# Performance work log

Measured on AMD Instinct MI355X. Metric: run time of the kernel, lower is better.

The kernel has to match this reference:

```python
import jax, jax.numpy as jnp
import numpy as np

D_MODEL = 96
D_STATE = 16
D_CONV = 3
D_INNER = 192          # expand * d_model
DT_RANK = 6            # ceil(d_model / 16)
K = 4                  # 4 scan directions
LN_EPS = 1e-5


def setup_inputs() -> dict:
    key = jax.random.key(0)
    ks = jax.random.split(key, 8)
    rn = lambda k, shape, s: jax.random.normal(k, shape, jnp.float32) * s
    return {
        "x": rn(ks[0], (8, 64, 64, D_MODEL), 1.0),
        "in_proj_w": rn(ks[1], (2 * D_INNER, D_MODEL), 0.05),
        "conv_w": rn(ks[2], (D_INNER, 1, D_CONV, D_CONV), 0.1),
        "conv_b": rn(ks[3], (D_INNER,), 0.1),
        "x_proj_w": rn(ks[4], (K * (DT_RANK + 2 * D_STATE), D_INNER), 0.05),
        "dt_projs_w": rn(ks[5], (K * D_INNER, DT_RANK), 0.1),
        "dt_projs_b": rn(ks[6], (K * D_INNER,), 0.1),
        "A_log": jnp.log(jnp.tile(jnp.arange(1, D_STATE + 1, dtype=jnp.float32), (D_INNER, 1))),
        "Ds": jnp.ones((K * D_INNER,), jnp.float32),
        "out_norm_w": jnp.ones((D_INNER,), jnp.float32),
        "out_norm_b": jnp.zeros((D_INNER,), jnp.float32),
        "out_proj_w": rn(ks[7], (D_MODEL, D_INNER), 0.05),
    }


def _selective_scan(u, delta, A, Bs, Cs):
    # u, delta: (B,K,D,L); A: (D,N); Bs, Cs: (B,K,N,L)
    Bsz = u.shape[0]

    def step(h, t):
        u_t, d_t, B_t, C_t = t                       # (B,K,D), (B,K,D), (B,K,N), (B,K,N)
        h = jnp.exp(d_t[..., None] * A) * h + (d_t * u_t)[..., None] * B_t[:, :, None, :]
        y = jnp.einsum('bkdn,bkn->bkd', h, C_t)
        return h, y

    h0 = jnp.zeros((Bsz, K, D_INNER, D_STATE), u.dtype)
    seq = (jnp.moveaxis(u, -1, 0), jnp.moveaxis(delta, -1, 0),
           jnp.moveaxis(Bs, -1, 0), jnp.moveaxis(Cs, -1, 0))
    _, ys = jax.lax.scan(step, h0, seq)
    return jnp.moveaxis(ys, 0, -1)                   # (B,K,D,L)


def reference(x, in_proj_w, conv_w, conv_b, x_proj_w, dt_projs_w, dt_projs_b,
              A_log, Ds, out_norm_w, out_norm_b, out_proj_w):
    B, H, W, C = x.shape
    L = H * W
    # in_proj + gate split
    xz = x @ in_proj_w.T                             # (B,H,W,2*D_INNER)
    x_, z = jnp.split(xz, 2, axis=-1)
    # depthwise conv + SiLU (NCHW)
    xc = jnp.transpose(x_, (0, 3, 1, 2))
    pad = (D_CONV - 1) // 2
    xc = jax.lax.conv_general_dilated(xc, conv_w, (1, 1), [(pad, pad), (pad, pad)],
                                      feature_group_count=D_INNER)
    xc = xc + conv_b[None, :, None, None]
    xc = xc * jax.nn.sigmoid(xc)
    # CrossScan: 4 directions
    x0 = xc.reshape(B, D_INNER, L)
    x1 = jnp.transpose(xc, (0, 1, 3, 2)).reshape(B, D_INNER, L)
    xs = jnp.stack([x0, x1, x0[..., ::-1], x1[..., ::-1]], axis=1)   # (B,4,D,L)
    # per-direction projections
    x_dbl = jnp.einsum('bkdl,kcd->bkcl', xs, x_proj_w.reshape(K, -1, D_INNER))
    dts, Bs, Cs = jnp.split(x_dbl, [DT_RANK, DT_RANK + D_STATE], axis=2)
    dts = jnp.einsum('bkrl,kdr->bkdl', dts, dt_projs_w.reshape(K, D_INNER, DT_RANK))
    delta = jax.nn.softplus(dts + dt_projs_b.reshape(1, K, D_INNER, 1))
    A = -jnp.exp(A_log)                              # (D,N), shared across K
    ys = _selective_scan(xs, delta, A, Bs, Cs)
    ys = ys + Ds.reshape(1, K, D_INNER, 1) * xs      # skip term D*u
    # CrossMerge
    y02 = ys[:, 0] + ys[:, 2, :, ::-1]
    y13 = ys[:, 1] + ys[:, 3, :, ::-1]
    y = y02 + jnp.transpose(y13.reshape(B, D_INNER, W, H), (0, 1, 3, 2)).reshape(B, D_INNER, L)
    # LayerNorm over channels (out_norm, 'v0' path)
    yt = jnp.transpose(y, (0, 2, 1))                 # (B,L,D)
    mu = yt.mean(-1, keepdims=True)
    var = yt.var(-1, keepdims=True)
    yt = (yt - mu) / jnp.sqrt(var + LN_EPS) * out_norm_w + out_norm_b
    yt = yt.reshape(B, H, W, D_INNER)
    # gate and out_proj
    yg = yt * (z * jax.nn.sigmoid(z))
    return yg @ out_proj_w.T
```

## Files before the change

### kernel.cpp

```cpp
#include <hip/hip_runtime.h>
#include <hip/hip_bf16.h>

typedef __hip_bfloat16 bf16;
typedef unsigned short u16;
typedef unsigned int   u32;

constexpr int Hn=64, Wn=64, Cm=96, Ln=4096, Di=192, Kn=4, Ns=16, Rr=6;
constexpr int Gc=64, CH=64;

typedef __attribute__((ext_vector_type(8))) short bf16x8;
typedef __attribute__((ext_vector_type(4))) float f32x4;

static __device__ __forceinline__ float ldv(const float* p, long i){ return p[i]; }
static __device__ __forceinline__ float ldv(const bf16*  p, long i){ return __bfloat162float(p[i]); }
static __device__ __forceinline__ void  stv(float* p, long i, float v){ p[i] = v; }
static __device__ __forceinline__ void  stv(bf16*  p, long i, float v){ p[i] = __float2bfloat16(v); }
static __device__ __forceinline__ float bfr(u16 u){ return __uint_as_float((u32)u << 16); }
static __device__ __forceinline__ u16   fbr(float f){ bf16 h = __float2bfloat16(f); return *(u16*)&h; }
static __device__ __forceinline__ float4 ldv4(const float* p, long i){ return *(const float4*)(p + i); }
static __device__ __forceinline__ float4 ldv4(const bf16* p, long i){
  ushort4 u = *(const ushort4*)(p + i);
  return make_float4(bfr(u.x), bfr(u.y), bfr(u.z), bfr(u.w));
}
static __device__ __forceinline__ float splus(float x){ return (x > 15.f) ? x : log1pf(__expf(x)); }

static __device__ __forceinline__ bf16x8 ldb8(const float* p){
  float4 a = *(const float4*)p;
  float4 b = *(const float4*)(p + 4);
  bf16x8 r;
  r[0]=(short)fbr(a.x); r[1]=(short)fbr(a.y); r[2]=(short)fbr(a.z); r[3]=(short)fbr(a.w);
  r[4]=(short)fbr(b.x); r[5]=(short)fbr(b.y); r[6]=(short)fbr(b.z); r[7]=(short)fbr(b.w);
  return r;
}
static __device__ __forceinline__ bf16x8 ldb8(const bf16* p){
  return *(const bf16x8*)p;
}
static __device__ __forceinline__ void st8(u16* dst, const float* src){
  float4 a = *(const float4*)src;
  float4 b = *(const float4*)(src + 4);
  dst[0]=fbr(a.x); dst[1]=fbr(a.y); dst[2]=fbr(a.z); dst[3]=fbr(a.w);
  dst[4]=fbr(b.x); dst[5]=fbr(b.y); dst[6]=fbr(b.z); dst[7]=fbr(b.w);
// ... 206 lines not shown
      int b  = (int)(q >> 12);
      int ql = (int)(q & 4095);
      int l  = (k >= 2) ? (4095 - ql) : ql;
      long base = ((long)(b*4 + k))*4096 + l;
      if (t < 6){
        dtsg[base*6 + t] = fbr(acc[f][r]);
      } else {
        int n = t - 6;
        u32 v = (u32)fbr(acc[f][r]) | ((u32)fbr(acc[f+1][r]) << 16);
        BCg[base*16 + n] = v;
      }
    }
  }
}
__global__ __launch_bounds__(256) void k_proj(const u16* xcLD, const u16* xcTLD, const void* xpw,
                                              u16* dtsg, u32* BCg, const int* flag){
  __shared__ u16 sA[64*200];
  if (*flag) proj_body<float>(xcLD, xcTLD, (const float*)xpw, dtsg, BCg, sA);
  else       proj_body<bf16 >(xcLD, xcTLD, (const bf16* )xpw, dtsg, BCg, sA);
}

static __device__ __forceinline__ void sp_decay(float xv, float& dl, float& rr){
  if (xv > 15.f){ dl = xv; rr = __expf(-xv); }
  else {
    float o = 1.f + __expf(xv);
    dl = __logf(o);
    rr = __builtin_amdgcn_rcpf(o);
  }
}

__global__ __launch_bounds__(192,3) void k_scan1_fast(const u16* xcLD, const u16* xcTLD,
                                                      const u16* dtsg, const u32* BCg,
                                                      const void* dtw, const void* dtb,
                                                      float* Sb, float* Qb,
                                                      const int* flag, const int* flag2){
  if (!(*flag && *flag2)) return;
  __shared__ float sdt[384];
  __shared__ float sB[1024];
  const float* dtwf = (const float*)dtw;
  const float* dtbf = (const float*)dtb;
  int tid = threadIdx.x, blk = blockIdx.x;
  int g = blk & (Gc-1); int k = (blk >> 6) & 3; int b = blk >> 8;
  bool rev = k >= 2, odd = k & 1;
  int d = tid;
  const u16* src = (odd ? xcTLD : xcLD) + (long)b*Ln*Di;
  const u16* dlg = dtsg + (long)(b*Kn + k)*Ln*6;
  const u32* bcg = BCg + (long)(b*Kn + k)*Ln*16;
  float w[6], h[16];
  #pragma unroll
  for (int r = 0; r < 6; ++r) w[r] = dtwf[((long)k*Di + d)*6 + r];
  float bias = dtbf[k*Di + d];
  #pragma unroll
  for (int n = 0; n < 16; ++n) h[n] = 0.f;
  float S = 0.f;
  int l0 = g*CH;
  for (int i = tid; i < 48; i += 192){
    const u16* sp8 = dlg + (long)l0*6 + i*8;
    ushort4 v0 = *(const ushort4*)sp8;
    ushort4 v1 = *(const ushort4*)(sp8 + 4);
    float* dp = &sdt[i*8];
    dp[0]=bfr(v0.x); dp[1]=bfr(v0.y); dp[2]=bfr(v0.z); dp[3]=bfr(v0.w);
    dp[4]=bfr(v1.x); dp[5]=bfr(v1.y); dp[6]=bfr(v1.z); dp[7]=bfr(v1.w);
  }
  for (int i = tid; i < 256; i += 192){
    uint4 v = *(const uint4*)(bcg + (long)l0*16 + i*4);
    sB[i*4+0] = bfr((u16)(v.x & 0xffff));
    sB[i*4+1] = bfr((u16)(v.y & 0xffff));
    sB[i*4+2] = bfr((u16)(v.z & 0xffff));
    sB[i*4+3] = bfr((u16)(v.w & 0xffff));
  }
  __syncthreads();
  for (int jb = 0; jb < CH; jb += 8){
    float uv[8];
    #pragma unroll
    for (int q = 0; q < 8; ++q){
      int l = l0 + jb + q; int pos = rev ? (Ln-1-l) : l;
      uv[q] = bfr(src[(long)pos*Di + d]);
    }
    #pragma unroll
    for (int q = 0; q < 8; ++q){
      int j = jb + q;
      float xv = bias;
      #pragma unroll
      for (int r = 0; r < 6; ++r) xv += w[r]*sdt[j*6 + r];
      float dl, rr; sp_decay(xv, dl, rr);
      float du = dl * uv[q];
      float Bv[16];
      *(float4*)&Bv[0]  = *(const float4*)&sB[j*16];
      *(float4*)&Bv[4]  = *(const float4*)&sB[j*16+4];
      *(float4*)&Bv[8]  = *(const float4*)&sB[j*16+8];
      *(float4*)&Bv[12] = *(const float4*)&sB[j*16+12];
      float r2 = rr*rr, r3 = r2*rr, r4 = r2*r2, r8 = r4*r4, r12 = r8*r4;
      float S4[4] = {rr, r2, r3, r4};
      float B4[4] = {1.f, r4, r8, r12};
      #pragma unroll
      for (int n = 0; n < 16; ++n)
        h[n] = (B4[n>>2]*S4[n&3])*h[n] + du*Bv[n];
      S += dl;
    }
  }
  long ci = (long)(b*Kn + k)*Gc + g;
  Sb[ci*Di + d] = S;
  float4* qp = (float4*)(Qb + ci*3072 + (long)d*16);
  qp[0] = make_float4(h[0], h[1], h[2], h[3]);
  qp[1] = make_float4(h[4], h[5], h[6], h[7]);
  qp[2] = make_float4(h[8], h[9], h[10], h[11]);
  qp[3] = make_float4(h[12], h[13], h[14], h[15]);
}

template<typename T>
__device__ void scan1_body(const u16* xcLD, const u16* xcTLD, const u16* dtsg, const u32* BCg,
                           const T* Alog, const T* dtw, const T* dtb,
                           float* Sb, float* Qb, float* sdt, float* sB, int fastA){
  int tid = threadIdx.x, blk = blockIdx.x;
  int g = blk & (Gc-1); int k = (blk >> 6) & 3; int b = blk >> 8;
  bool rev = k >= 2, odd = k & 1;
  int d = tid;
  const u16* src = (odd ? xcTLD : xcLD) + (long)b*Ln*Di;
  const u16* dlg = dtsg + (long)(b*Kn + k)*Ln*6;
  const u32* bcg = BCg + (long)(b*Kn + k)*Ln*16;
  float w[6], h[16], a[16];
  #pragma unroll
  for (int r = 0; r < 6; ++r) w[r] = ldv(dtw, ((long)k*Di + d)*6 + r);
  float bias = ldv(dtb, k*Di + d);
  #pragma unroll
  for (int n = 0; n < 16; ++n) h[n] = 0.f;
  if (!fastA){
    #pragma unroll
    for (int n = 0; n < 16; ++n) a[n] = -__expf(ldv(Alog, (long)d*16 + n));
  }
  float S = 0.f;
  int l0 = g*CH;
  for (int i = tid; i < 48; i += 192){
    const u16* sp8 = dlg + (long)l0*6 + i*8;
    ushort4 v0 = *(const ushort4*)sp8;
    ushort4 v1 = *(const ushort4*)(sp8 + 4);
    float* dp = &sdt[i*8];
    dp[0]=bfr(v0.x); dp[1]=bfr(v0.y); dp[2]=bfr(v0.z); dp[3]=bfr(v0.w);
    dp[4]=bfr(v1.x); dp[5]=bfr(v1.y); dp[6]=bfr(v1.z); dp[7]=bfr(v1.w);
  }
  for (int i = tid; i < 256; i += 192){
    uint4 v = *(const uint4*)(bcg + (long)l0*16 + i*4);
    sB[i*4+0] = bfr((u16)(v.x & 0xffff));
    sB[i*4+1] = bfr((u16)(v.y & 0xffff));
    sB[i*4+2] = bfr((u16)(v.z & 0xffff));
    sB[i*4+3] = bfr((u16)(v.w & 0xffff));
  }
  __syncthreads();
  if (fastA){
    for (int jb = 0; jb < CH; jb += 8){
      float uv[8];
      #pragma unroll
      for (int q = 0; q < 8; ++q){
        int l = l0 + jb + q; int pos = rev ? (Ln-1-l) : l;
        uv[q] = bfr(src[(long)pos*Di + d]);
      }
      #pragma unroll
      for (int q = 0; q < 8; ++q){
        int j = jb + q;
        float xv = bias;
        #pragma unroll
        for (int r = 0; r < 6; ++r) xv += w[r]*sdt[j*6 + r];
        float dl, rr; sp_decay(xv, dl, rr);
        float du = dl * uv[q];
        float Bv[16];
        *(float4*)&Bv[0]  = *(const float4*)&sB[j*16];
        *(float4*)&Bv[4]  = *(const float4*)&sB[j*16+4];
        *(float4*)&Bv[8]  = *(const float4*)&sB[j*16+8];
        *(float4*)&Bv[12] = *(const float4*)&sB[j*16+12];
        float r2 = rr*rr, r3 = r2*rr, r4 = r2*r2, r8 = r4*r4, r12 = r8*r4;
        float S4[4] = {rr, r2, r3, r4};
        float B4[4] = {1.f, r4, r8, r12};
        #pragma unroll
        for (int n = 0; n < 16; ++n)
          h[n] = (B4[n>>2]*S4[n&3])*h[n] + du*Bv[n];
        S += dl;
      }
    }
  } else {
    for (int jb = 0; jb < CH; jb += 8){
      float uv[8];
      #pragma unroll
      for (int q = 0; q < 8; ++q){
        int l = l0 + jb + q; int pos = rev ? (Ln-1-l) : l;
        uv[q] = bfr(src[(long)pos*Di + d]);
      }
      #pragma unroll
      for (int q = 0; q < 8; ++q){
        int j = jb + q;
        float dl = bias;
        #pragma unroll
        for (int r = 0; r < 6; ++r) dl += w[r]*sdt[j*6 + r];
        dl = splus(dl);
        float du = dl * uv[q];
        float Bv[16];
        *(float4*)&Bv[0]  = *(const float4*)&sB[j*16];
        *(float4*)&Bv[4]  = *(const float4*)&sB[j*16+4];
        *(float4*)&Bv[8]  = *(const float4*)&sB[j*16+8];
        *(float4*)&Bv[12] = *(const float4*)&sB[j*16+12];
        #pragma unroll
        for (int n = 0; n < 16; ++n) h[n] = __expf(dl*a[n])*h[n] + du*Bv[n];
        S += dl;
      }
    }
  }
  long ci = (long)(b*Kn + k)*Gc + g;
  Sb[ci*Di + d] = S;
  float4* qp = (float4*)(Qb + ci*3072 + (long)d*16);
  qp[0] = make_float4(h[0], h[1], h[2], h[3]);
  qp[1] = make_float4(h[4], h[5], h[6], h[7]);
  qp[2] = make_float4(h[8], h[9], h[10], h[11]);
  qp[3] = make_float4(h[12], h[13], h[14], h[15]);
}
__global__ __launch_bounds__(192,3) void k_scan1_gen(const u16* xcLD, const u16* xcTLD, const u16* dtsg,
                                                     const u32* BCg, const void* Alog, const void* dtw,
                                                     const void* dtb, float* Sb, float* Qb,
                                                     const int* flag, const int* flag2){
  __shared__ float sdt[384];
  __shared__ float sB[1024];
  int f = *flag, f2 = *flag2;
  if (f && f2) return;
  if (f) scan1_body<float>(xcLD, xcTLD, dtsg, BCg, (const float*)Alog, (const float*)dtw,
                           (const float*)dtb, Sb, Qb, sdt, sB, f2);
  else   scan1_body<bf16 >(xcLD, xcTLD, dtsg, BCg, (const bf16* )Alog, (const bf16* )dtw,
                           (const bf16* )dtb, Sb, Qb, sdt, sB, f2);
}

template<typename T>
__device__ void fix_body(const float* Sb, const float* Qb, const T* Alog, float* Hin){
  int bk = blockIdx.x >> 2, qr = blockIdx.x & 3;
  int s0 = qr*768 + threadIdx.x;
  float aa[3], hh[3];
  #pragma unroll
  for (int q = 0; q < 3; ++q){
    int s = s0 + 256*q;
    aa[q] = -__expf(ldv(Alog, s));
    hh[q] = 0.f;
  }
  for (int g = 0; g < Gc; ++g){
    long ci = (long)bk*Gc + g;
    #pragma unroll
    for (int q = 0; q < 3; ++q){
      int s = s0 + 256*q;
      Hin[ci*3072 + s] = hh[q];
      hh[q] = __expf(aa[q]*Sb[ci*Di + (s >> 4)])*hh[q] + Qb[ci*3072 + s];
    }
  }
}
__global__ __launch_bounds__(256) void k_fix(const float* Sb, const float* Qb, const void* Alog,
                                             float* Hin, const int* flag){
  if (*flag) fix_body<float>(Sb, Qb, (const float*)Alog, Hin);
  else       fix_body<bf16 >(Sb, Qb, (const bf16* )Alog, Hin);
}

__global__ __launch_bounds__(192,3) void k_scan2_fast(const u16* xcLD, const u16* xcTLD,
                                                      const u16* dtsg, const u32* BCg,
                                                      const void* dtw, const void* dtb,
                                                      const float* Hin, u16* ys,
                                                      const int* flag, const int* flag2){
  if (!(*flag && *flag2)) return;
  __shared__ float sdt[384];
  __shared__ float sB[1024];
  __shared__ float sC[1024];
  const float* dtwf = (const float*)dtw;
  const float* dtbf = (const float*)dtb;
  int tid = threadIdx.x, blk = blockIdx.x;
  int g = blk & (Gc-1); int k = (blk >> 6) & 3; int b = blk >> 8;
  bool rev = k >= 2, odd = k & 1;
  int d = tid;
  const u16* src = (odd ? xcTLD : xcLD) + (long)b*Ln*Di;
  const u16* dlg = dtsg + (long)(b*Kn + k)*Ln*6;
  const u32* bcg = BCg + (long)(b*Kn + k)*Ln*16;
  u16* yb = ys + (long)(b*Kn + k)*Ln*Di;
  float w[6], h[16];
  #pragma unroll
  for (int r = 0; r < 6; ++r) w[r] = dtwf[((long)k*Di + d)*6 + r];
  float bias = dtbf[k*Di + d];
  long ci = (long)(b*Kn + k)*Gc + g;
  {
    const float4* hp = (const float4*)(Hin + ci*3072 + (long)d*16);
    float4 h0 = hp[0], h1 = hp[1], h2 = hp[2], h3 = hp[3];
    h[0]=h0.x; h[1]=h0.y; h[2]=h0.z; h[3]=h0.w;
    h[4]=h1.x; h[5]=h1.y; h[6]=h1.z; h[7]=h1.w;
    h[8]=h2.x; h[9]=h2.y; h[10]=h2.z; h[11]=h2.w;
    h[12]=h3.x; h[13]=h3.y; h[14]=h3.z; h[15]=h3.w;
  }
  int l0 = g*CH;
  for (int i = tid; i < 48; i += 192){
    const u16* sp8 = dlg + (long)l0*6 + i*8;
    ushort4 v0 = *(const ushort4*)sp8;
    ushort4 v1 = *(const ushort4*)(sp8 + 4);
    float* dp = &sdt[i*8];
    dp[0]=bfr(v0.x); dp[1]=bfr(v0.y); dp[2]=bfr(v0.z); dp[3]=bfr(v0.w);
    dp[4]=bfr(v1.x); dp[5]=bfr(v1.y); dp[6]=bfr(v1.z); dp[7]=bfr(v1.w);
  }
  for (int i = tid; i < 256; i += 192){
    uint4 v = *(const uint4*)(bcg + (long)l0*16 + i*4);
    sB[i*4+0] = bfr((u16)(v.x & 0xffff)); sC[i*4+0] = bfr((u16)(v.x >> 16));
    sB[i*4+1] = bfr((u16)(v.y & 0xffff)); sC[i*4+1] = bfr((u16)(v.y >> 16));
    sB[i*4+2] = bfr((u16)(v.z & 0xffff)); sC[i*4+2] = bfr((u16)(v.z >> 16));
    sB[i*4+3] = bfr((u16)(v.w & 0xffff)); sC[i*4+3] = bfr((u16)(v.w >> 16));
  }
  __syncthreads();
  for (int jb = 0; jb < CH; jb += 8){
    float uv[8];
    #pragma unroll
    for (int q = 0; q < 8; ++q){
      int l = l0 + jb + q; int pos = rev ? (Ln-1-l) : l;
      uv[q] = bfr(src[(long)pos*Di + d]);
    }
    #pragma unroll
    for (int q = 0; q < 8; ++q){
      int j = jb + q;
      float xv = bias;
      #pragma unroll
      for (int r = 0; r < 6; ++r) xv += w[r]*sdt[j*6 + r];
      float dl, rr; sp_decay(xv, dl, rr);
      float du = dl * uv[q];
      float Bv[16], Cv[16];
      *(float4*)&Bv[0]  = *(const float4*)&sB[j*16];
      *(float4*)&Bv[4]  = *(const float4*)&sB[j*16+4];
      *(float4*)&Bv[8]  = *(const float4*)&sB[j*16+8];
      *(float4*)&Bv[12] = *(const float4*)&sB[j*16+12];
      *(float4*)&Cv[0]  = *(const float4*)&sC[j*16];
      *(float4*)&Cv[4]  = *(const float4*)&sC[j*16+4];
      *(float4*)&Cv[8]  = *(const float4*)&sC[j*16+8];
      *(float4*)&Cv[12] = *(const float4*)&sC[j*16+12];
      float r2 = rr*rr, r3 = r2*rr, r4 = r2*r2, r8 = r4*r4, r12 = r8*r4;
      float S4[4] = {rr, r2, r3, r4};
      float B4[4] = {1.f, r4, r8, r12};
      float y = 0.f;
      #pragma unroll
      for (int n = 0; n < 16; ++n){
        h[n] = (B4[n>>2]*S4[n&3])*h[n] + du*Bv[n];
        y += h[n]*Cv[n];
      }
      int l = l0 + j; int le = rev ? (Ln-1-l) : l;
      int sp = odd ? ((le & 63)*64 + (le >> 6)) : le;
      yb[(long)sp*Di + d] = fbr(y);
    }
  }
}

template<typename T>
__device__ void scan2_body(const u16* xcLD, const u16* xcTLD, const u16* dtsg, const u32* BCg,
                           const T* Alog, const T* dtw, const T* dtb, const float* Hin,
                           u16* ys, float* sdt, float* sB, float* sC, int fastA){
  int tid = threadIdx.x, blk = blockIdx.x;
  int g = blk & (Gc-1); int k = (blk >> 6) & 3; int b = blk >> 8;
  bool rev = k >= 2, odd = k & 1;
  int d = tid;
  const u16* src = (odd ? xcTLD : xcLD) + (long)b*Ln*Di;
  const u16* dlg = dtsg + (long)(b*Kn + k)*Ln*6;
  const u32* bcg = BCg + (long)(b*Kn + k)*Ln*16;
  u16* yb = ys + (long)(b*Kn + k)*Ln*Di;
  float w[6], h[16], a[16];
  #pragma unroll
  for (int r = 0; r < 6; ++r) w[r] = ldv(dtw, ((long)k*Di + d)*6 + r);
  float bias = ldv(dtb, k*Di + d);
  long ci = (long)(b*Kn + k)*Gc + g;
  {
    const float4* hp = (const float4*)(Hin + ci*3072 + (long)d*16);
    float4 h0 = hp[0], h1 = hp[1], h2 = hp[2], h3 = hp[3];
    h[0]=h0.x; h[1]=h0.y; h[2]=h0.z; h[3]=h0.w;
    h[4]=h1.x; h[5]=h1.y; h[6]=h1.z; h[7]=h1.w;
    h[8]=h2.x; h[9]=h2.y; h[10]=h2.z; h[11]=h2.w;
    h[12]=h3.x; h[13]=h3.y; h[14]=h3.z; h[15]=h3.w;
  }
  if (!fastA){
    #pragma unroll
    for (int n = 0; n < 16; ++n) a[n] = -__expf(ldv(Alog, (long)d*16 + n));
  }
  int l0 = g*CH;
  for (int i = tid; i < 48; i += 192){
    const u16* sp8 = dlg + (long)l0*6 + i*8;
    ushort4 v0 = *(const ushort4*)sp8;
    ushort4 v1 = *(const ushort4*)(sp8 + 4);
    float* dp = &sdt[i*8];
    dp[0]=bfr(v0.x); dp[1]=bfr(v0.y); dp[2]=bfr(v0.z); dp[3]=bfr(v0.w);
    dp[4]=bfr(v1.x); dp[5]=bfr(v1.y); dp[6]=bfr(v1.z); dp[7]=bfr(v1.w);
  }
  for (int i = tid; i < 256; i += 192){
    uint4 v = *(const uint4*)(bcg + (long)l0*16 + i*4);
    sB[i*4+0] = bfr((u16)(v.x & 0xffff)); sC[i*4+0] = bfr((u16)(v.x >> 16));
    sB[i*4+1] = bfr((u16)(v.y & 0xffff)); sC[i*4+1] = bfr((u16)(v.y >> 16));
    sB[i*4+2] = bfr((u16)(v.z & 0xffff)); sC[i*4+2] = bfr((u16)(v.z >> 16));
    sB[i*4+3] = bfr((u16)(v.w & 0xffff)); sC[i*4+3] = bfr((u16)(v.w >> 16));
  }
  __syncthreads();
  if (fastA){
    for (int jb = 0; jb < CH; jb += 8){
      float uv[8];
      #pragma unroll
      for (int q = 0; q < 8; ++q){
        int l = l0 + jb + q; int pos = rev ? (Ln-1-l) : l;
        uv[q] = bfr(src[(long)pos*Di + d]);
      }
      #pragma unroll
      for (int q = 0; q < 8; ++q){
        int j = jb + q;
        float xv = bias;
        #pragma unroll
        for (int r = 0; r < 6; ++r) xv += w[r]*sdt[j*6 + r];
        float dl, rr; sp_decay(xv, dl, rr);
        float du = dl * uv[q];
        float Bv[16], Cv[16];
        *(float4*)&Bv[0]  = *(const float4*)&sB[j*16];
        *(float4*)&Bv[4]  = *(const float4*)&sB[j*16+4];
        *(float4*)&Bv[8]  = *(const float4*)&sB[j*16+8];
        *(float4*)&Bv[12] = *(const float4*)&sB[j*16+12];
        *(float4*)&Cv[0]  = *(const float4*)&sC[j*16];
        *(float4*)&Cv[4]  = *(const float4*)&sC[j*16+4];
        *(float4*)&Cv[8]  = *(const float4*)&sC[j*16+8];
        *(float4*)&Cv[12] = *(const float4*)&sC[j*16+12];
        float r2 = rr*rr, r3 = r2*rr, r4 = r2*r2, r8 = r4*r4, r12 = r8*r4;
        float S4[4] = {rr, r2, r3, r4};
        float B4[4] = {1.f, r4, r8, r12};
        float y = 0.f;
        #pragma unroll
        for (int n = 0; n < 16; ++n){
          h[n] = (B4[n>>2]*S4[n&3])*h[n] + du*Bv[n];
          y += h[n]*Cv[n];
        }
        int l = l0 + j; int le = rev ? (Ln-1-l) : l;
        int sp = odd ? ((le & 63)*64 + (le >> 6)) : le;
        yb[(long)sp*Di + d] = fbr(y);
      }
    }
  } else {
    for (int jb = 0; jb < CH; jb += 8){
      float uv[8];
      #pragma unroll
      for (int q = 0; q < 8; ++q){
        int l = l0 + jb + q; int pos = rev ? (Ln-1-l) : l;
        uv[q] = bfr(src[(long)pos*Di + d]);
      }
      #pragma unroll
      for (int q = 0; q < 8; ++q){
        int j = jb + q;
        float dl = bias;
        #pragma unroll
        for (int r = 0; r < 6; ++r) dl += w[r]*sdt[j*6 + r];
        dl = splus(dl);
        float du = dl * uv[q];
        float Bv[16], Cv[16];
        *(float4*)&Bv[0]  = *(const float4*)&sB[j*16];
        *(float4*)&Bv[4]  = *(const float4*)&sB[j*16+4];
        *(float4*)&Bv[8]  = *(const float4*)&sB[j*16+8];
        *(float4*)&Bv[12] = *(const float4*)&sB[j*16+12];
        *(float4*)&Cv[0]  = *(const float4*)&sC[j*16];
        *(float4*)&Cv[4]  = *(const float4*)&sC[j*16+4];
        *(float4*)&Cv[8]  = *(const float4*)&sC[j*16+8];
        *(float4*)&Cv[12] = *(const float4*)&sC[j*16+12];
        float y = 0.f;
        #pragma unroll
        for (int n = 0; n < 16; ++n){
          h[n] = __expf(dl*a[n])*h[n] + du*Bv[n];
          y += h[n]*Cv[n];
        }
        int l = l0 + j; int le = rev ? (Ln-1-l) : l;
        int sp = odd ? ((le & 63)*64 + (le >> 6)) : le;
        yb[(long)sp*Di + d] = fbr(y);
      }
    }
  }
}
__global__ __launch_bounds__(192,3) void k_scan2_gen(const u16* xcLD, const u16* xcTLD, const u16* dtsg,
                                                     const u32* BCg, const void* Alog, const void* dtw,
                                                     const void* dtb, const float* Hin, u16* ys,
                                                     const int* flag, const int* flag2){
  __shared__ float sdt[384];
  __shared__ float sB[1024];
  __shared__ float sC[1024];
  int f = *flag, f2 = *flag2;
  if (f && f2) return;
  if (f) scan2_body<float>(xcLD, xcTLD, dtsg, BCg, (const float*)Alog, (const float*)dtw,
                           (const float*)dtb, Hin, ys, sdt, sB, sC, f2);
  else   scan2_body<bf16 >(xcLD, xcTLD, dtsg, BCg, (const bf16* )Alog, (const bf16* )dtw,
                           (const bf16* )dtb, Hin, ys, sdt, sB, sC, f2);
}

template<typename T>
__device__ void out_body(const u16* ys, const u16* xcLD, const u16* Z, const T* Dsv,
                         const T* lnw, const T* lnb, const T* wo, T* out, long obase,
                         u16* ty, float* sDs){
  int blk = blockIdx.x;
  int b = blk >> 7; int rem = blk & 127; int h = rem >> 1; int half = rem & 1;
  int tid = threadIdx.x;
  int p0 = h*64 + half*32;
  const u16* xcb = xcLD + (long)b*Ln*Di;
  const u16* Zb  = Z + (long)b*Ln*Di;
  const u16* pl0 = ys + (long)(b*Kn + 0)*Ln*Di;
  const u16* pl1 = ys + (long)(b*Kn + 1)*Ln*Di;
// ... 68 lines not shown
}
__global__ __launch_bounds__(256) void k_out(const u16* ys, const u16* xcLD, const u16* Z,
                                             const void* Dsv, const void* lnw, const void* lnb,
                                             const void* wo, void* out, long obase, const int* flag){
  __shared__ u16 ty[32*200];
  __shared__ float sDs[Di];
  if (*flag) out_body<float>(ys, xcLD, Z, (const float*)Dsv, (const float*)lnw, (const float*)lnb,
                             (const float*)wo, (float*)out, obase, ty, sDs);
  else       out_body<bf16 >(ys, xcLD, Z, (const bf16* )Dsv, (const bf16* )lnw, (const bf16* )lnb,
                             (const bf16* )wo, (bf16* )out, obase, ty, sDs);
}

extern "C" void kernel_launch(void* const* d_in, const int* in_sizes, int n_in,
                              void* d_out, int out_size, void* d_ws, size_t ws_size,
                              hipStream_t stream){
  const void* x    = d_in[0];
  const void* ipw  = d_in[1];
  const void* cw   = d_in[2];
  const void* cb   = d_in[3];
  const void* xpw  = d_in[4];
  const void* dtw  = d_in[5];
  const void* dtb  = d_in[6];
  const void* Alog = d_in[7];
  const void* Dsv  = d_in[8];
  const void* lnw  = d_in[9];
  const void* lnb  = d_in[10];
  const void* wo   = d_in[11];

  const size_t PLANE = (size_t)Ln*Di*2;
  const size_t YSB   = (size_t)Kn*Ln*Di*2;
  const size_t SBB   = (size_t)Kn*Gc*Di*4;
  const size_t QBB   = (size_t)Kn*Gc*Di*Ns*4;
  const size_t HIB   = QBB;
  const size_t perB  = 4*PLANE + YSB + SBB + QBB + HIB;
  int Bc = 1;
  for (int c : {8, 4, 2, 1}) if (256 + (size_t)c*perB <= ws_size){ Bc = c; break; }
  int nch = 8 / Bc;

  char* base = (char*)d_ws;
  int*  flag  = (int*)base;
  int*  flag2 = (int*)(base + 8);
  u16* Z     = (u16*)(base + 256);
  u16* xcLD  = Z     + (size_t)Bc*Ln*Di;
  u16* xcTLD = xcLD  + (size_t)Bc*Ln*Di;
  u16* Xb    = xcTLD + (size_t)Bc*Ln*Di;
  u16* ys    = Xb    + (size_t)Bc*Ln*Di;
  float* Sb  = (float*)(ys + (size_t)Bc*Kn*Ln*Di);
  float* Qb  = Sb + (size_t)Bc*Kn*Gc*Di;
  float* Hin = Qb + (size_t)Bc*Kn*Gc*Di*Ns;
  u16* dts   = Xb;
  u32* BC    = (u32*)(dts + (size_t)Bc*Kn*Ln*6);

  k_detect<<<1, 256, 0, stream>>>((const u16*)x, Alog, flag, flag2);

  for (int ch = 0; ch < nch; ++ch){
    long xoff = (long)ch*Bc*Ln*Cm;
    k_inproj <<<Bc*Ln/64,     256, 0, stream>>>(x, xoff, ipw, Xb, Z, flag);
    k_conv   <<<Bc*Hn*3,      256, 0, stream>>>(Xb, cw, cb, xcLD, xcTLD, flag);
    k_proj   <<<Bc*(Ln/64)*2, 256, 0, stream>>>(xcLD, xcTLD, xpw, dts, BC, flag);
    k_scan1_fast<<<Bc*Kn*Gc,  192, 0, stream>>>(xcLD, xcTLD, dts, BC, dtw, dtb, Sb, Qb, flag, flag2);
    k_scan1_gen <<<Bc*Kn*Gc,  192, 0, stream>>>(xcLD, xcTLD, dts, BC, Alog, dtw, dtb, Sb, Qb, flag, flag2);
    k_fix    <<<Bc*Kn*4,      256, 0, stream>>>(Sb, Qb, Alog, Hin, flag);
    k_scan2_fast<<<Bc*Kn*Gc,  192, 0, stream>>>(xcLD, xcTLD, dts, BC, dtw, dtb, Hin, ys, flag, flag2);
    k_scan2_gen <<<Bc*Kn*Gc,  192, 0, stream>>>(xcLD, xcTLD, dts, BC, Alog, dtw, dtb, Hin, ys, flag, flag2);
    k_out    <<<Bc*Hn*2,      256, 0, stream>>>(ys, xcLD, Z, Dsv, lnw, lnb, wo, d_out, xoff, flag);
  }
}
```

Measured before the change: 352.4 us.

## Halve scan chunk count and cache softplus delta between scan passes

The chunked scan now uses 32 chunks of 128 steps, processed as two 64-step tiles, instead of 64 chunks of 64. This halves the carry-state traffic and the work in the chunk-fix pass. The fast first pass also writes the softplus delta to a new fp32 workspace buffer, so the second pass reads it and recomputes only exp(-delta) instead of redoing the dt projection and softplus. The cost is a large extra fp32 write and read per element, more workspace that may force smaller batch chunks, and half as many blocks in flight.

```diff
diff --git a/kernel.cpp b/kernel.cpp
--- a/kernel.cpp
+++ b/kernel.cpp
@@ -6,7 +6,7 @@
 typedef unsigned int   u32;
 
 constexpr int Hn=64, Wn=64, Cm=96, Ln=4096, Di=192, Kn=4, Ns=16, Rr=6;
-constexpr int Gc=64, CH=64;
+constexpr int Gc=32, CH=128;
 
 typedef __attribute__((ext_vector_type(8))) short bf16x8;
 typedef __attribute__((ext_vector_type(4))) float f32x4;
@@ -279,7 +279,7 @@
 __global__ __launch_bounds__(192,3) void k_scan1_fast(const u16* xcLD, const u16* xcTLD,
                                                       const u16* dtsg, const u32* BCg,
                                                       const void* dtw, const void* dtb,
-                                                      float* Sb, float* Qb,
+                                                      float* Sb, float* Qb, float* Aux,
                                                       const int* flag, const int* flag2){
   if (!(*flag && *flag2)) return;
   __shared__ float sdt[384];
@@ -287,12 +287,13 @@
   const float* dtwf = (const float*)dtw;
   const float* dtbf = (const float*)dtb;
   int tid = threadIdx.x, blk = blockIdx.x;
-  int g = blk & (Gc-1); int k = (blk >> 6) & 3; int b = blk >> 8;
+  int g = blk & (Gc-1); int k = (blk >> 5) & 3; int b = blk >> 7;
   bool rev = k >= 2, odd = k & 1;
   int d = tid;
   const u16* src = (odd ? xcTLD : xcLD) + (long)b*Ln*Di;
   const u16* dlg = dtsg + (long)(b*Kn + k)*Ln*6;
   const u32* bcg = BCg + (long)(b*Kn + k)*Ln*16;
+  float* auxb = Aux + (long)(b*Kn + k)*Ln*Di;
   float w[6], h[16];
   #pragma unroll
   for (int r = 0; r < 6; ++r) w[r] = dtwf[((long)k*Di + d)*6 + r];
@@ -301,105 +302,30 @@
   for (int n = 0; n < 16; ++n) h[n] = 0.f;
   float S = 0.f;
   int l0 = g*CH;
-  for (int i = tid; i < 48; i += 192){
-    const u16* sp8 = dlg + (long)l0*6 + i*8;
-    ushort4 v0 = *(const ushort4*)sp8;
-    ushort4 v1 = *(const ushort4*)(sp8 + 4);
-    float* dp = &sdt[i*8];
-    dp[0]=bfr(v0.x); dp[1]=bfr(v0.y); dp[2]=bfr(v0.z); dp[3]=bfr(v0.w);
-    dp[4]=bfr(v1.x); dp[5]=bfr(v1.y); dp[6]=bfr(v1.z); dp[7]=bfr(v1.w);
-  }
-  for (int i = tid; i < 256; i += 192){
-    uint4 v = *(const uint4*)(bcg + (long)l0*16 + i*4);
-    sB[i*4+0] = bfr((u16)(v.x & 0xffff));
-    sB[i*4+1] = bfr((u16)(v.y & 0xffff));
-    sB[i*4+2] = bfr((u16)(v.z & 0xffff));
-    sB[i*4+3] = bfr((u16)(v.w & 0xffff));
-  }
-  __syncthreads();
-  for (int jb = 0; jb < CH; jb += 8){
-    float uv[8];
-    #pragma unroll
-    for (int q = 0; q < 8; ++q){
-      int l = l0 + jb + q; int pos = rev ? (Ln-1-l) : l;
-      uv[q] = bfr(src[(long)pos*Di + d]);
-    }
-    #pragma unroll
-    for (int q = 0; q < 8; ++q){
-      int j = jb + q;
-      float xv = bias;
-      #pragma unroll
-      for (int r = 0; r < 6; ++r) xv += w[r]*sdt[j*6 + r];
-      float dl, rr; sp_decay(xv, dl, rr);
-      float du = dl * uv[q];
-      float Bv[16];
-      *(float4*)&Bv[0]  = *(const float4*)&sB[j*16];
-      *(float4*)&Bv[4]  = *(const float4*)&sB[j*16+4];
-      *(float4*)&Bv[8]  = *(const float4*)&sB[j*16+8];
-      *(float4*)&Bv[12] = *(const float4*)&sB[j*16+12];
-      float r2 = rr*rr, r3 = r2*rr, r4 = r2*r2, r8 = r4*r4, r12 = r8*r4;
-      float S4[4] = {rr, r2, r3, r4};
-      float B4[4] = {1.f, r4, r8, r12};
-      #pragma unroll
-      for (int n = 0; n < 16; ++n)
-        h[n] = (B4[n>>2]*S4[n&3])*h[n] + du*Bv[n];
-      S += dl;
-    }
-  }
-  long ci = (long)(b*Kn + k)*Gc + g;
-  Sb[ci*Di + d] = S;
-  float4* qp = (float4*)(Qb + ci*3072 + (long)d*16);
-  qp[0] = make_float4(h[0], h[1], h[2], h[3]);
-  qp[1] = make_float4(h[4], h[5], h[6], h[7]);
-  qp[2] = make_float4(h[8], h[9], h[10], h[11]);
-  qp[3] = make_float4(h[12], h[13], h[14], h[15]);
-}
-
-template<typename T>
-__device__ void scan1_body(const u16* xcLD, const u16* xcTLD, const u16* dtsg, const u32* BCg,
-                           const T* Alog, const T* dtw, const T* dtb,
-                           float* Sb, float* Qb, float* sdt, float* sB, int fastA){
-  int tid = threadIdx.x, blk = blockIdx.x;
-  int g = blk & (Gc-1); int k = (blk >> 6) & 3; int b = blk >> 8;
-  bool rev = k >= 2, odd = k & 1;
-  int d = tid;
-  const u16* src = (odd ? xcTLD : xcLD) + (long)b*Ln*Di;
-  const u16* dlg = dtsg + (long)(b*Kn + k)*Ln*6;
-  const u32* bcg = BCg + (long)(b*Kn + k)*Ln*16;
-  float w[6], h[16], a[16];
-  #pragma unroll
-  for (int r = 0; r < 6; ++r) w[r] = ldv(dtw, ((long)k*Di + d)*6 + r);
-  float bias = ldv(dtb, k*Di + d);
-  #pragma unroll
-  for (int n = 0; n < 16; ++n) h[n] = 0.f;
-  if (!fastA){
-    #pragma unroll
-    for (int n = 0; n < 16; ++n) a[n] = -__expf(ldv(Alog, (long)d*16 + n));
-  }
-  float S = 0.f;
-  int l0 = g*CH;
-  for (int i = tid; i < 48; i += 192){
-    const u16* sp8 = dlg + (long)l0*6 + i*8;
-    ushort4 v0 = *(const ushort4*)sp8;
-    ushort4 v1 = *(const ushort4*)(sp8 + 4);
-    float* dp = &sdt[i*8];
-    dp[0]=bfr(v0.x); dp[1]=bfr(v0.y); dp[2]=bfr(v0.z); dp[3]=bfr(v0.w);
-    dp[4]=bfr(v1.x); dp[5]=bfr(v1.y); dp[6]=bfr(v1.z); dp[7]=bfr(v1.w);
-  }
-  for (int i = tid; i < 256; i += 192){
-    uint4 v = *(const uint4*)(bcg + (long)l0*16 + i*4);
-    sB[i*4+0] = bfr((u16)(v.x & 0xffff));
-    sB[i*4+1] = bfr((u16)(v.y & 0xffff));
-    sB[i*4+2] = bfr((u16)(v.z & 0xffff));
-    sB[i*4+3] = bfr((u16)(v.w & 0xffff));
-  }
-  __syncthreads();
-  if (fastA){
-    for (int jb = 0; jb < CH; jb += 8){
+  for (int t = 0; t < 2; ++t){
+    int lt = l0 + t*64;
+    __syncthreads();
+    for (int i = tid; i < 48; i += 192){
+      const u16* sp8 = dlg + (long)lt*6 + i*8;
+      ushort4 v0 = *(const ushort4*)sp8;
+      ushort4 v1 = *(const ushort4*)(sp8 + 4);
+      float* dp = &sdt[i*8];
+      dp[0]=bfr(v0.x); dp[1]=bfr(v0.y); dp[2]=bfr(v0.z); dp[3]=bfr(v0.w);
+      dp[4]=bfr(v1.x); dp[5]=bfr(v1.y); dp[6]=bfr(v1.z); dp[7]=bfr(v1.w);
+    }
+    for (int i = tid; i < 256; i += 192){
+      uint4 v = *(const uint4*)(bcg + (long)lt*16 + i*4);
+      sB[i*4+0] = bfr((u16)(v.x & 0xffff));
+      sB[i*4+1] = bfr((u16)(v.y & 0xffff));
+      sB[i*4+2] = bfr((u16)(v.z & 0xffff));
+      sB[i*4+3] = bfr((u16)(v.w & 0xffff));
+    }
+    __syncthreads();
+    for (int jb = 0; jb < 64; jb += 8){
       float uv[8];
       #pragma unroll
       for (int q = 0; q < 8; ++q){
-        int l = l0 + jb + q; int pos = rev ? (Ln-1-l) : l;
+        int l = lt + jb + q; int pos = rev ? (Ln-1-l) : l;
         uv[q] = bfr(src[(long)pos*Di + d]);
       }
       #pragma unroll
@@ -409,6 +335,7 @@
         #pragma unroll
         for (int r = 0; r < 6; ++r) xv += w[r]*sdt[j*6 + r];
         float dl, rr; sp_decay(xv, dl, rr);
+        auxb[(long)(lt + j)*Di + d] = dl;
         float du = dl * uv[q];
         float Bv[16];
         *(float4*)&Bv[0]  = *(const float4*)&sB[j*16];
@@ -424,12 +351,63 @@
         S += dl;
       }
     }
-  } else {
-    for (int jb = 0; jb < CH; jb += 8){
+  }
+  long ci = (long)(b*Kn + k)*Gc + g;
+  Sb[ci*Di + d] = S;
+  float4* qp = (float4*)(Qb + ci*3072 + (long)d*16);
+  qp[0] = make_float4(h[0], h[1], h[2], h[3]);
+  qp[1] = make_float4(h[4], h[5], h[6], h[7]);
+  qp[2] = make_float4(h[8], h[9], h[10], h[11]);
+  qp[3] = make_float4(h[12], h[13], h[14], h[15]);
+}
+
+template<typename T>
+__device__ void scan1_body(const u16* xcLD, const u16* xcTLD, const u16* dtsg, const u32* BCg,
+                           const T* Alog, const T* dtw, const T* dtb,
+                           float* Sb, float* Qb, float* sdt, float* sB, int fastA){
+  int tid = threadIdx.x, blk = blockIdx.x;
+  int g = blk & (Gc-1); int k = (blk >> 5) & 3; int b = blk >> 7;
+  bool rev = k >= 2, odd = k & 1;
+  int d = tid;
+  const u16* src = (odd ? xcTLD : xcLD) + (long)b*Ln*Di;
+  const u16* dlg = dtsg + (long)(b*Kn + k)*Ln*6;
+  const u32* bcg = BCg + (long)(b*Kn + k)*Ln*16;
+  float w[6], h[16], a[16];
+  #pragma unroll
+  for (int r = 0; r < 6; ++r) w[r] = ldv(dtw, ((long)k*Di + d)*6 + r);
+  float bias = ldv(dtb, k*Di + d);
+  #pragma unroll
+  for (int n = 0; n < 16; ++n) h[n] = 0.f;
+  if (!fastA){
+    #pragma unroll
+    for (int n = 0; n < 16; ++n) a[n] = -__expf(ldv(Alog, (long)d*16 + n));
+  }
+  float S = 0.f;
+  int l0 = g*CH;
+  for (int t = 0; t < 2; ++t){
+    int lt = l0 + t*64;
+    __syncthreads();
+    for (int i = tid; i < 48; i += 192){
+      const u16* sp8 = dlg + (long)lt*6 + i*8;
+      ushort4 v0 = *(const ushort4*)sp8;
+      ushort4 v1 = *(const ushort4*)(sp8 + 4);
+      float* dp = &sdt[i*8];
+      dp[0]=bfr(v0.x); dp[1]=bfr(v0.y); dp[2]=bfr(v0.z); dp[3]=bfr(v0.w);
+      dp[4]=bfr(v1.x); dp[5]=bfr(v1.y); dp[6]=bfr(v1.z); dp[7]=bfr(v1.w);
+    }
+    for (int i = tid; i < 256; i += 192){
+      uint4 v = *(const uint4*)(bcg + (long)lt*16 + i*4);
+      sB[i*4+0] = bfr((u16)(v.x & 0xffff));
+      sB[i*4+1] = bfr((u16)(v.y & 0xffff));
+      sB[i*4+2] = bfr((u16)(v.z & 0xffff));
+      sB[i*4+3] = bfr((u16)(v.w & 0xffff));
+    }
+    __syncthreads();
+    for (int jb = 0; jb < 64; jb += 8){
       float uv[8];
       #pragma unroll
       for (int q = 0; q < 8; ++q){
-        int l = l0 + jb + q; int pos = rev ? (Ln-1-l) : l;
+        int l = lt + jb + q; int pos = rev ? (Ln-1-l) : l;
         uv[q] = bfr(src[(long)pos*Di + d]);
       }
       #pragma unroll
@@ -438,15 +416,26 @@
         float dl = bias;
         #pragma unroll
         for (int r = 0; r < 6; ++r) dl += w[r]*sdt[j*6 + r];
-        dl = splus(dl);
+        float rr = 0.f;
+        if (fastA){ float xv = dl; sp_decay(xv, dl, rr); }
+        else dl = splus(dl);
         float du = dl * uv[q];
         float Bv[16];
         *(float4*)&Bv[0]  = *(const float4*)&sB[j*16];
         *(float4*)&Bv[4]  = *(const float4*)&sB[j*16+4];
         *(float4*)&Bv[8]  = *(const float4*)&sB[j*16+8];
         *(float4*)&Bv[12] = *(const float4*)&sB[j*16+12];
-        #pragma unroll
-        for (int n = 0; n < 16; ++n) h[n] = __expf(dl*a[n])*h[n] + du*Bv[n];
+        if (fastA){
+          float r2 = rr*rr, r3 = r2*rr, r4 = r2*r2, r8 = r4*r4, r12 = r8*r4;
+          float S4[4] = {rr, r2, r3, r4};
+          float B4[4] = {1.f, r4, r8, r12};
+          #pragma unroll
+          for (int n = 0; n < 16; ++n)
+            h[n] = (B4[n>>2]*S4[n&3])*h[n] + du*Bv[n];
+        } else {
+          #pragma unroll
+          for (int n = 0; n < 16; ++n) h[n] = __expf(dl*a[n])*h[n] + du*Bv[n];
+        }
         S += dl;
       }
     }
@@ -501,28 +490,21 @@
 }
 
 __global__ __launch_bounds__(192,3) void k_scan2_fast(const u16* xcLD, const u16* xcTLD,
-                                                      const u16* dtsg, const u32* BCg,
-                                                      const void* dtw, const void* dtb,
-                                                      const float* Hin, u16* ys,
+                                                      const u32* BCg, const float* Hin,
+                                                      const float* Aux, u16* ys,
                                                       const int* flag, const int* flag2){
   if (!(*flag && *flag2)) return;
-  __shared__ float sdt[384];
   __shared__ float sB[1024];
   __shared__ float sC[1024];
-  const float* dtwf = (const float*)dtw;
-  const float* dtbf = (const float*)dtb;
   int tid = threadIdx.x, blk = blockIdx.x;
-  int g = blk & (Gc-1); int k = (blk >> 6) & 3; int b = blk >> 8;
+  int g = blk & (Gc-1); int k = (blk >> 5) & 3; int b = blk >> 7;
   bool rev = k >= 2, odd = k & 1;
   int d = tid;
   const u16* src = (odd ? xcTLD : xcLD) + (long)b*Ln*Di;
-  const u16* dlg = dtsg + (long)(b*Kn + k)*Ln*6;
   const u32* bcg = BCg + (long)(b*Kn + k)*Ln*16;
+  const float* auxb = Aux + (long)(b*Kn + k)*Ln*Di;
   u16* yb = ys + (long)(b*Kn + k)*Ln*Di;
-  float w[6], h[16];
-  #pragma unroll
-  for (int r = 0; r < 6; ++r) w[r] = dtwf[((long)k*Di + d)*6 + r];
-  float bias = dtbf[k*Di + d];
+  float h[16];
   long ci = (long)(b*Kn + k)*Gc + g;
   {
     const float4* hp = (const float4*)(Hin + ci*3072 + (long)d*16);
@@ -533,123 +515,30 @@
     h[12]=h3.x; h[13]=h3.y; h[14]=h3.z; h[15]=h3.w;
   }
   int l0 = g*CH;
-  for (int i = tid; i < 48; i += 192){
-    const u16* sp8 = dlg + (long)l0*6 + i*8;
-    ushort4 v0 = *(const ushort4*)sp8;
-    ushort4 v1 = *(const ushort4*)(sp8 + 4);
-    float* dp = &sdt[i*8];
-    dp[0]=bfr(v0.x); dp[1]=bfr(v0.y); dp[2]=bfr(v0.z); dp[3]=bfr(v0.w);
-    dp[4]=bfr(v1.x); dp[5]=bfr(v1.y); dp[6]=bfr(v1.z); dp[7]=bfr(v1.w);
-  }
-  for (int i = tid; i < 256; i += 192){
-    uint4 v = *(const uint4*)(bcg + (long)l0*16 + i*4);
-    sB[i*4+0] = bfr((u16)(v.x & 0xffff)); sC[i*4+0] = bfr((u16)(v.x >> 16));
-    sB[i*4+1] = bfr((u16)(v.y & 0xffff)); sC[i*4+1] = bfr((u16)(v.y >> 16));
-    sB[i*4+2] = bfr((u16)(v.z & 0xffff)); sC[i*4+2] = bfr((u16)(v.z >> 16));
-    sB[i*4+3] = bfr((u16)(v.w & 0xffff)); sC[i*4+3] = bfr((u16)(v.w >> 16));
-  }
-  __syncthreads();
-  for (int jb = 0; jb < CH; jb += 8){
-    float uv[8];
-    #pragma unroll
-    for (int q = 0; q < 8; ++q){
-      int l = l0 + jb + q; int pos = rev ? (Ln-1-l) : l;
-      uv[q] = bfr(src[(long)pos*Di + d]);
-    }
-    #pragma unroll
-    for (int q = 0; q < 8; ++q){
-      int j = jb + q;
-      float xv = bias;
-      #pragma unroll
-      for (int r = 0; r < 6; ++r) xv += w[r]*sdt[j*6 + r];
-      float dl, rr; sp_decay(xv, dl, rr);
-      float du = dl * uv[q];
-      float Bv[16], Cv[16];
-      *(float4*)&Bv[0]  = *(const float4*)&sB[j*16];
-      *(float4*)&Bv[4]  = *(const float4*)&sB[j*16+4];
-      *(float4*)&Bv[8]  = *(const float4*)&sB[j*16+8];
-      *(float4*)&Bv[12] = *(const float4*)&sB[j*16+12];
-      *(float4*)&Cv[0]  = *(const float4*)&sC[j*16];
-      *(float4*)&Cv[4]  = *(const float4*)&sC[j*16+4];
-      *(float4*)&Cv[8]  = *(const float4*)&sC[j*16+8];
-      *(float4*)&Cv[12] = *(const float4*)&sC[j*16+12];
-      float r2 = rr*rr, r3 = r2*rr, r4 = r2*r2, r8 = r4*r4, r12 = r8*r4;
-      float S4[4] = {rr, r2, r3, r4};
-      float B4[4] = {1.f, r4, r8, r12};
-      float y = 0.f;
-      #pragma unroll
-      for (int n = 0; n < 16; ++n){
-        h[n] = (B4[n>>2]*S4[n&3])*h[n] + du*Bv[n];
-        y += h[n]*Cv[n];
-      }
-      int l = l0 + j; int le = rev ? (Ln-1-l) : l;
-      int sp = odd ? ((le & 63)*64 + (le >> 6)) : le;
-      yb[(long)sp*Di + d] = fbr(y);
-    }
-  }
-}
-
-template<typename T>
-__device__ void scan2_body(const u16* xcLD, const u16* xcTLD, const u16* dtsg, const u32* BCg,
-                           const T* Alog, const T* dtw, const T* dtb, const float* Hin,
-                           u16* ys, float* sdt, float* sB, float* sC, int fastA){
-  int tid = threadIdx.x, blk = blockIdx.x;
-  int g = blk & (Gc-1); int k = (blk >> 6) & 3; int b = blk >> 8;
-  bool rev = k >= 2, odd = k & 1;
-  int d = tid;
-  const u16* src = (odd ? xcTLD : xcLD) + (long)b*Ln*Di;
-  const u16* dlg = dtsg + (long)(b*Kn + k)*Ln*6;
-  const u32* bcg = BCg + (long)(b*Kn + k)*Ln*16;
-  u16* yb = ys + (long)(b*Kn + k)*Ln*Di;
-  float w[6], h[16], a[16];
-  #pragma unroll
-  for (int r = 0; r < 6; ++r) w[r] = ldv(dtw, ((long)k*Di + d)*6 + r);
-  float bias = ldv(dtb, k*Di + d);
-  long ci = (long)(b*Kn + k)*Gc + g;
-  {
-    const float4* hp = (const float4*)(Hin + ci*3072 + (long)d*16);
-    float4 h0 = hp[0], h1 = hp[1], h2 = hp[2], h3 = hp[3];
-    h[0]=h0.x; h[1]=h0.y; h[2]=h0.z; h[3]=h0.w;
-    h[4]=h1.x; h[5]=h1.y; h[6]=h1.z; h[7]=h1.w;
-    h[8]=h2.x; h[9]=h2.y; h[10]=h2.z; h[11]=h2.w;
-    h[12]=h3.x; h[13]=h3.y; h[14]=h3.z; h[15]=h3.w;
-  }
-  if (!fastA){
-    #pragma unroll
-    for (int n = 0; n < 16; ++n) a[n] = -__expf(ldv(Alog, (long)d*16 + n));
-  }
-  int l0 = g*CH;
-  for (int i = tid; i < 48; i += 192){
-    const u16* sp8 = dlg + (long)l0*6 + i*8;
-    ushort4 v0 = *(const ushort4*)sp8;
-    ushort4 v1 = *(const ushort4*)(sp8 + 4);
-    float* dp = &sdt[i*8];
-    dp[0]=bfr(v0.x); dp[1]=bfr(v0.y); dp[2]=bfr(v0.z); dp[3]=bfr(v0.w);
-    dp[4]=bfr(v1.x); dp[5]=bfr(v1.y); dp[6]=bfr(v1.z); dp[7]=bfr(v1.w);
-  }
-  for (int i = tid; i < 256; i += 192){
-    uint4 v = *(const uint4*)(bcg + (long)l0*16 + i*4);
-    sB[i*4+0] = bfr((u16)(v.x & 0xffff)); sC[i*4+0] = bfr((u16)(v.x >> 16));
-    sB[i*4+1] = bfr((u16)(v.y & 0xffff)); sC[i*4+1] = bfr((u16)(v.y >> 16));
-    sB[i*4+2] = bfr((u16)(v.z & 0xffff)); sC[i*4+2] = bfr((u16)(v.z >> 16));
-    sB[i*4+3] = bfr((u16)(v.w & 0xffff)); sC[i*4+3] = bfr((u16)(v.w >> 16));
-  }
-  __syncthreads();
-  if (fastA){
-    for (int jb = 0; jb < CH; jb += 8){
-      float uv[8];
+  for (int t = 0; t < 2; ++t){
+    int lt = l0 + t*64;
+    __syncthreads();
+    for (int i = tid; i < 256; i += 192){
+      uint4 v = *(const uint4*)(bcg + (long)lt*16 + i*4);
+      sB[i*4+0] = bfr((u16)(v.x & 0xffff)); sC[i*4+0] = bfr((u16)(v.x >> 16));
+      sB[i*4+1] = bfr((u16)(v.y & 0xffff)); sC[i*4+1] = bfr((u16)(v.y >> 16));
+      sB[i*4+2] = bfr((u16)(v.z & 0xffff)); sC[i*4+2] = bfr((u16)(v.z >> 16));
+      sB[i*4+3] = bfr((u16)(v.w & 0xffff)); sC[i*4+3] = bfr((u16)(v.w >> 16));
+    }
+    __syncthreads();
+    for (int jb = 0; jb < 64; jb += 8){
+      float uv[8], dlv[8];
       #pragma unroll
       for (int q = 0; q < 8; ++q){
-        int l = l0 + jb + q; int pos = rev ? (Ln-1-l) : l;
-        uv[q] = bfr(src[(long)pos*Di + d]);
+        int l = lt + jb + q; int pos = rev ? (Ln-1-l) : l;
+        uv[q]  = bfr(src[(long)pos*Di + d]);
+        dlv[q] = auxb[(long)l*Di + d];
       }
       #pragma unroll
       for (int q = 0; q < 8; ++q){
         int j = jb + q;
-        float xv = bias;
-        #pragma unroll
-        for (int r = 0; r < 6; ++r) xv += w[r]*sdt[j*6 + r];
-        float dl, rr; sp_decay(xv, dl, rr);
+        float dl = dlv[q];
+        float rr = __expf(-dl);
         float du = dl * uv[q];
         float Bv[16], Cv[16];
         *(float4*)&Bv[0]  = *(const float4*)&sB[j*16];
@@ -669,17 +558,68 @@
           h[n] = (B4[n>>2]*S4[n&3])*h[n] + du*Bv[n];
           y += h[n]*Cv[n];
         }
-        int l = l0 + j; int le = rev ? (Ln-1-l) : l;
+        int l = lt + j; int le = rev ? (Ln-1-l) : l;
         int sp = odd ? ((le & 63)*64 + (le >> 6)) : le;
         yb[(long)sp*Di + d] = fbr(y);
       }
     }
-  } else {
-    for (int jb = 0; jb < CH; jb += 8){
+  }
+}
+
+template<typename T>
+__device__ void scan2_body(const u16* xcLD, const u16* xcTLD, const u16* dtsg, const u32* BCg,
+                           const T* Alog, const T* dtw, const T* dtb, const float* Hin,
+                           u16* ys, float* sdt, float* sB, float* sC, int fastA){
+  int tid = threadIdx.x, blk = blockIdx.x;
+  int g = blk & (Gc-1); int k = (blk >> 5) & 3; int b = blk >> 7;
+  bool rev = k >= 2, odd = k & 1;
+  int d = tid;
+  const u16* src = (odd ? xcTLD : xcLD) + (long)b*Ln*Di;
+  const u16* dlg = dtsg + (long)(b*Kn + k)*Ln*6;
+  const u32* bcg = BCg + (long)(b*Kn + k)*Ln*16;
+  u16* yb = ys + (long)(b*Kn + k)*Ln*Di;
+  float w[6], h[16], a[16];
+  #pragma unroll
+  for (int r = 0; r < 6; ++r) w[r] = ldv(dtw, ((long)k*Di + d)*6 + r);
+  float bias = ldv(dtb, k*Di + d);
+  long ci = (long)(b*Kn + k)*Gc + g;
+  {
+    const float4* hp = (const float4*)(Hin + ci*3072 + (long)d*16);
+    float4 h0 = hp[0], h1 = hp[1], h2 = hp[2], h3 = hp[3];
+    h[0]=h0.x; h[1]=h0.y; h[2]=h0.z; h[3]=h0.w;
+    h[4]=h1.x; h[5]=h1.y; h[6]=h1.z; h[7]=h1.w;
+    h[8]=h2.x; h[9]=h2.y; h[10]=h2.z; h[11]=h2.w;
+    h[12]=h3.x; h[13]=h3.y; h[14]=h3.z; h[15]=h3.w;
+  }
+  if (!fastA){
+    #pragma unroll
+    for (int n = 0; n < 16; ++n) a[n] = -__expf(ldv(Alog, (long)d*16 + n));
+  }
+  int l0 = g*CH;
+  for (int t = 0; t < 2; ++t){
+    int lt = l0 + t*64;
+    __syncthreads();
+    for (int i = tid; i < 48; i += 192){
+      const u16* sp8 = dlg + (long)lt*6 + i*8;
+      ushort4 v0 = *(const ushort4*)sp8;
+      ushort4 v1 = *(const ushort4*)(sp8 + 4);
+      float* dp = &sdt[i*8];
+      dp[0]=bfr(v0.x); dp[1]=bfr(v0.y); dp[2]=bfr(v0.z); dp[3]=bfr(v0.w);
+      dp[4]=bfr(v1.x); dp[5]=bfr(v1.y); dp[6]=bfr(v1.z); dp[7]=bfr(v1.w);
+    }
+    for (int i = tid; i < 256; i += 192){
+      uint4 v = *(const uint4*)(bcg + (long)lt*16 + i*4);
+      sB[i*4+0] = bfr((u16)(v.x & 0xffff)); sC[i*4+0] = bfr((u16)(v.x >> 16));
+      sB[i*4+1] = bfr((u16)(v.y & 0xffff)); sC[i*4+1] = bfr((u16)(v.y >> 16));
+      sB[i*4+2] = bfr((u16)(v.z & 0xffff)); sC[i*4+2] = bfr((u16)(v.z >> 16));
+      sB[i*4+3] = bfr((u16)(v.w & 0xffff)); sC[i*4+3] = bfr((u16)(v.w >> 16));
+    }
+    __syncthreads();
+    for (int jb = 0; jb < 64; jb += 8){
       float uv[8];
       #pragma unroll
       for (int q = 0; q < 8; ++q){
-        int l = l0 + jb + q; int pos = rev ? (Ln-1-l) : l;
+        int l = lt + jb + q; int pos = rev ? (Ln-1-l) : l;
         uv[q] = bfr(src[(long)pos*Di + d]);
       }
       #pragma unroll
@@ -688,7 +628,9 @@
         float dl = bias;
         #pragma unroll
         for (int r = 0; r < 6; ++r) dl += w[r]*sdt[j*6 + r];
-        dl = splus(dl);
+        float rr = 0.f;
+        if (fastA){ float xv = dl; sp_decay(xv, dl, rr); }
+        else dl = splus(dl);
         float du = dl * uv[q];
         float Bv[16], Cv[16];
         *(float4*)&Bv[0]  = *(const float4*)&sB[j*16];
@@ -700,12 +642,23 @@
         *(float4*)&Cv[8]  = *(const float4*)&sC[j*16+8];
         *(float4*)&Cv[12] = *(const float4*)&sC[j*16+12];
         float y = 0.f;
-        #pragma unroll
-        for (int n = 0; n < 16; ++n){
-          h[n] = __expf(dl*a[n])*h[n] + du*Bv[n];
-          y += h[n]*Cv[n];
+        if (fastA){
+          float r2 = rr*rr, r3 = r2*rr, r4 = r2*r2, r8 = r4*r4, r12 = r8*r4;
+          float S4[4] = {rr, r2, r3, r4};
+          float B4[4] = {1.f, r4, r8, r12};
+          #pragma unroll
+          for (int n = 0; n < 16; ++n){
+            h[n] = (B4[n>>2]*S4[n&3])*h[n] + du*Bv[n];
+            y += h[n]*Cv[n];
+          }
+        } else {
+          #pragma unroll
+          for (int n = 0; n < 16; ++n){
+            h[n] = __expf(dl*a[n])*h[n] + du*Bv[n];
+            y += h[n]*Cv[n];
+          }
         }
-        int l = l0 + j; int le = rev ? (Ln-1-l) : l;
+        int l = lt + j; int le = rev ? (Ln-1-l) : l;
         int sp = odd ? ((le & 63)*64 + (le >> 6)) : le;
         yb[(long)sp*Di + d] = fbr(y);
       }
@@ -840,7 +793,8 @@
   const size_t SBB   = (size_t)Kn*Gc*Di*4;
   const size_t QBB   = (size_t)Kn*Gc*Di*Ns*4;
   const size_t HIB   = QBB;
-  const size_t perB  = 4*PLANE + YSB + SBB + QBB + HIB;
+  const size_t AXB   = (size_t)Kn*Ln*Di*4;
+  const size_t perB  = 4*PLANE + YSB + SBB + QBB + HIB + AXB;
   int Bc = 1;
   for (int c : {8, 4, 2, 1}) if (256 + (size_t)c*perB <= ws_size){ Bc = c; break; }
   int nch = 8 / Bc;
@@ -856,6 +810,7 @@
   float* Sb  = (float*)(ys + (size_t)Bc*Kn*Ln*Di);
   float* Qb  = Sb + (size_t)Bc*Kn*Gc*Di;
   float* Hin = Qb + (size_t)Bc*Kn*Gc*Di*Ns;
+  float* Aux = Hin + (size_t)Bc*Kn*Gc*Di*Ns;
   u16* dts   = Xb;
   u32* BC    = (u32*)(dts + (size_t)Bc*Kn*Ln*6);
 
@@ -866,10 +821,10 @@
     k_inproj <<<Bc*Ln/64,     256, 0, stream>>>(x, xoff, ipw, Xb, Z, flag);
     k_conv   <<<Bc*Hn*3,      256, 0, stream>>>(Xb, cw, cb, xcLD, xcTLD, flag);
     k_proj   <<<Bc*(Ln/64)*2, 256, 0, stream>>>(xcLD, xcTLD, xpw, dts, BC, flag);
-    k_scan1_fast<<<Bc*Kn*Gc,  192, 0, stream>>>(xcLD, xcTLD, dts, BC, dtw, dtb, Sb, Qb, flag, flag2);
+    k_scan1_fast<<<Bc*Kn*Gc,  192, 0, stream>>>(xcLD, xcTLD, dts, BC, dtw, dtb, Sb, Qb, Aux, flag, flag2);
     k_scan1_gen <<<Bc*Kn*Gc,  192, 0, stream>>>(xcLD, xcTLD, dts, BC, Alog, dtw, dtb, Sb, Qb, flag, flag2);
     k_fix    <<<Bc*Kn*4,      256, 0, stream>>>(Sb, Qb, Alog, Hin, flag);
-    k_scan2_fast<<<Bc*Kn*Gc,  192, 0, stream>>>(xcLD, xcTLD, dts, BC, dtw, dtb, Hin, ys, flag, flag2);
+    k_scan2_fast<<<Bc*Kn*Gc,  192, 0, stream>>>(xcLD, xcTLD, BC, Hin, Aux, ys, flag, flag2);
     k_scan2_gen <<<Bc*Kn*Gc,  192, 0, stream>>>(xcLD, xcTLD, dts, BC, Alog, dtw, dtb, Hin, ys, flag, flag2);
     k_out    <<<Bc*Hn*2,      256, 0, stream>>>(ys, xcLD, Z, Dsv, lnw, lnb, wo, d_out, xoff, flag);
   }
```

Result: slower. 398.7 us (+13.2%).
